# Kernel optimization log

Measured on AMD Instinct MI355X. Metric: run time of the kernel, lower is better.

The kernel has to match this reference:

```python
import jax, jax.numpy as jnp
import numpy as np


def setup_inputs() -> dict:
    key = jax.random.key(0)
    kq, kk, kv = jax.random.split(key, 3)
    B, S, D = 4, 4096, 256
    return {
        "query": jax.random.normal(kq, (B, S, D), dtype=jnp.float32),
        "key": jax.random.normal(kk, (B, S, D), dtype=jnp.float32),
        "value": jax.random.normal(kv, (B, S, D), dtype=jnp.float32),
    }


def reference(query, key, value):
    # Chunked attention with full softmax over keys per query chunk is
    # mathematically identical to standard scaled dot-product attention.
    dim = query.shape[-1]
    scale = 1.0 / jnp.sqrt(jnp.asarray(dim, query.dtype))
    scores = jnp.einsum("bqd,bkd->bqk", query, key) * scale  # (B, S, S)
    attn = jax.nn.softmax(scores, axis=-1)
    return jnp.einsum("bqk,bkd->bqd", attn, value)  # (B, S, D)
```

## Files before the change

kernel.cpp:

```cpp
#include <hip/hip_runtime.h>
#include <hip/hip_bf16.h>

#define B_ 4
#define S_ 4096
#define D_ 256
#define BM 128
#define BN 32
#define NSPLIT 4
#define SKEYS (S_/NSPLIT)
#define ITERS (SKEYS/BN)

typedef short v8s __attribute__((ext_vector_type(8)));
typedef float v16f __attribute__((ext_vector_type(16)));
typedef unsigned int v4u __attribute__((ext_vector_type(4)));

__device__ __forceinline__ unsigned short f2bf(float x){
    unsigned int u = __float_as_uint(x);
    u += 0x7fffu + ((u >> 16) & 1u);
    return (unsigned short)(u >> 16);
}
__device__ __forceinline__ unsigned int pkb(float a, float b){
    __hip_bfloat162 h = __float22bfloat162_rn(make_float2(a, b));
    union { __hip_bfloat162 h; unsigned int u; } c; c.h = h;
    return c.u;
}
__device__ __forceinline__ float bf2f(unsigned int lo16){
    return __uint_as_float(lo16 << 16);
}
__device__ __forceinline__ void gload_lds(const unsigned short* g, unsigned short* l){
    __builtin_amdgcn_global_load_lds(
        (const __attribute__((address_space(1))) unsigned int*)g,
        (__attribute__((address_space(3))) unsigned int*)l, 16, 0, 0);
}

__global__ void cvt_all(const float* __restrict__ q, const float* __restrict__ k,
                        const float* __restrict__ v,
                        uint4* __restrict__ qb, uint4* __restrict__ kb,
                        uint4* __restrict__ vt){
    __shared__ __align__(16) unsigned short lds[8192];
    int bx = blockIdx.x;
    int t  = threadIdx.x;
    int which = bx >> 9;
    int tile  = bx & 511;
    const float* srcm = (which == 0) ? q : (which == 1) ? k : v;
    const float4* src = (const float4*)(srcm + (size_t)tile * 8192);

    if (which < 2){
        const float sc = (which == 0) ? 0.09016994f : 1.0f;
        #pragma unroll
        for (int p = 0; p < 8; ++p){
            int i = p*256 + t;
            float4 a = src[i];
            int row = i >> 6, d0 = (i & 63) * 4;
            unsigned byte = (unsigned)(row*512 + d0*2) ^ (unsigned)((row & 7) << 4);
            uint2 u; u.x = pkb(a.x*sc, a.y*sc); u.y = pkb(a.z*sc, a.w*sc);
            *(uint2*)((char*)lds + byte) = u;
        }
        __syncthreads();
        uint4* dst = ((which == 0) ? qb : kb) + (size_t)tile * 1024;
        #pragma unroll
        for (int q4 = 0; q4 < 4; ++q4){
            int o = q4*256 + t;
            int c = o >> 5, row = o & 31;
            unsigned byte = (unsigned)(row*512 + c*16) ^ (unsigned)((row & 7) << 4);
            dst[o] = *(const uint4*)((const char*)lds + byte);
        }
    } else {
        #pragma unroll
        for (int p = 0; p < 8; ++p){
            int i = p*256 + t;
            float4 a = src[i];
            uint2 u; u.x = pkb(a.x, a.y); u.y = pkb(a.z, a.w);
            *(uint2*)((char*)lds + (size_t)i*8) = u;
        }
        __syncthreads();
        uint4* dst = vt + (size_t)tile * 1024;
        #pragma unroll
        for (int q4 = 0; q4 < 4; ++q4){
            union { unsigned short sh[8]; uint4 u; } cell;
            #pragma unroll
            for (int j = 0; j < 8; ++j)
                cell.sh[j] = lds[(q4*8 + j)*256 + t];
            dst[q4*256 + t] = cell.u;
        }
    }
}

__global__ __launch_bounds__(256, 2) void fa_main(
    const unsigned short* __restrict__ qb, const unsigned short* __restrict__ kb,
    const unsigned short* __restrict__ vtg,
    unsigned short* __restrict__ opart, float* __restrict__ lsep)
{
    __shared__ __align__(16) unsigned short sbuf[32768];

    int bid = blockIdx.x;
    int grp = bid & 15;
    int qt  = bid >> 4;
    int b = grp >> 2, split = grp & 3;
    int tid = threadIdx.x;
    int w = tid >> 6, lane = tid & 63, hi = lane >> 5, ln = lane & 31;

    const unsigned short* kg = (const unsigned short*)kb
                             + ((size_t)(b*128 + split*32))*8192;
    const unsigned short* vg = vtg + ((size_t)(b*128 + split*32))*8192;

    auto stageK = [&](int tile, int buf){
        const unsigned short* src = kg + (size_t)tile*8192 + w*2048;
        #pragma unroll
        for (int p = 0; p < 4; ++p)
            gload_lds(src + p*512 + lane*8, &sbuf[buf*8192 + w*2048 + p*512 + lane*8]);
    };
    auto stageV = [&](int tile, int buf){
        const unsigned short* src = vg + (size_t)tile*8192 + w*2048;
        #pragma unroll
        for (int p = 0; p < 4; ++p)
            gload_lds(src + p*512 + lane*8, &sbuf[16384 + buf*8192 + w*2048 + p*512 + lane*8]);
    };

    v8s qf[16];
    {
        const unsigned short* qsrc = qb + ((size_t)(b*128 + qt*4 + w))*8192;
        #pragma unroll
        for (int f = 0; f < 16; ++f)
            qf[f] = *(const v8s*)&qsrc[(2*f + hi)*256 + ln*8];
    }
    stageK(0, 0);
    stageV(0, 0);
    asm volatile("s_waitcnt vmcnt(0)" ::: "memory");
    __builtin_amdgcn_sched_barrier(0);
    __builtin_amdgcn_s_barrier();

    v16f oacc[8];
    #pragma unroll
    for (int t = 0; t < 8; ++t)
        #pragma unroll
        for (int r = 0; r < 16; ++r) oacc[t][r] = 0.0f;
    float l_run = 0.0f;
    v8s pf_prev[2] = {};

    for (int it = 0; it < ITERS; ++it){
        int cur = it & 1;
        const unsigned short* Kb    = &sbuf[cur*8192];
        const unsigned short* Vprev = &sbuf[16384 + (cur ^ 1)*8192];

        if (it + 1 < ITERS) stageK(it + 1, cur ^ 1);

        v16f sa, sb;
        #pragma unroll
        for (int r = 0; r < 16; ++r){ sa[r] = 0.0f; sb[r] = 0.0f; }
        __builtin_amdgcn_s_setprio(1);
        #pragma unroll
        for (int f = 0; f < 8; ++f){
            v8s a0 = *(const v8s*)&Kb[(2*f      + hi)*256 + ln*8];
            v8s a1 = *(const v8s*)&Kb[(2*(f+8) + hi)*256 + ln*8];
            sa = __builtin_amdgcn_mfma_f32_32x32x16_bf16(a0, qf[f],   sa, 0, 0, 0);
            sb = __builtin_amdgcn_mfma_f32_32x32x16_bf16(a1, qf[f+8], sb, 0, 0, 0);
        }
        __builtin_amdgcn_s_setprio(0);
        v16f sc2;
        #pragma unroll
        for (int r = 0; r < 16; ++r) sc2[r] = sa[r] + sb[r];

        if (it > 0){
            __builtin_amdgcn_s_setprio(1);
            #pragma unroll
            for (int ks = 0; ks < 2; ++ks){
                const unsigned short* vrow = &Vprev[(2*ks + hi)*2048 + ln*8];
                #pragma unroll
                for (int t2 = 0; t2 < 8; ++t2){
                    v8s av = *(const v8s*)&vrow[t2*256];
                    oacc[t2] = __builtin_amdgcn_mfma_f32_32x32x16_bf16(av, pf_prev[ks], oacc[t2], 0, 0, 0);
                }
            }
            __builtin_amdgcn_s_setprio(0);
        }

        __builtin_amdgcn_s_barrier();
        if (it + 1 < ITERS) stageV(it + 1, cur ^ 1);

        float ls = 0.0f;
        uint2 pA[4];
        #pragma unroll
        for (int c = 0; c < 4; ++c){
            float e0 = exp2f(sc2[4*c+0]), e1 = exp2f(sc2[4*c+1]);
            float e2 = exp2f(sc2[4*c+2]), e3 = exp2f(sc2[4*c+3]);
            ls += (e0 + e1) + (e2 + e3);
            pA[c].x = pkb(e0, e1); pA[c].y = pkb(e2, e3);
        }
        ls += __shfl_xor(ls, 32);
        l_run += ls;

        #pragma unroll
        for (int ks = 0; ks < 2; ++ks){
            uint2 snd = pA[2*ks + 1 - hi];
            uint2 rcv;
            rcv.x = (unsigned int)__shfl_xor((int)snd.x, 32);
            rcv.y = (unsigned int)__shfl_xor((int)snd.y, 32);
            uint2 lo = hi ? rcv : pA[2*ks];
            uint2 hb = hi ? pA[2*ks+1] : rcv;
            union { unsigned int u[4]; v8s v; } cc;
            cc.u[0] = lo.x; cc.u[1] = lo.y; cc.u[2] = hb.x; cc.u[3] = hb.y;
            pf_prev[ks] = cc.v;
        }

        if (it == ITERS - 1) asm volatile("s_waitcnt vmcnt(0)" ::: "memory");
        else                 asm volatile("s_waitcnt vmcnt(4)" ::: "memory");
        __builtin_amdgcn_sched_barrier(0);
        __builtin_amdgcn_s_barrier();
    }

    {
        const unsigned short* Vlast = &sbuf[16384 + ((ITERS - 1) & 1)*8192];
        __builtin_amdgcn_s_setprio(1);
        #pragma unroll
        for (int ks = 0; ks < 2; ++ks){
            const unsigned short* vrow = &Vlast[(2*ks + hi)*2048 + ln*8];
            #pragma unroll
            for (int t2 = 0; t2 < 8; ++t2){
                v8s av = *(const v8s*)&vrow[t2*256];
                oacc[t2] = __builtin_amdgcn_mfma_f32_32x32x16_bf16(av, pf_prev[ks], oacc[t2], 0, 0, 0);
            }
        }
        __builtin_amdgcn_s_setprio(0);
    }

    float inv = 1.0f / l_run;
    size_t orow0 = (size_t)(split*B_ + b)*S_ + qt*BM + w*32;
    if (hi == 0) lsep[orow0 + ln] = l_run;

    unsigned short* myreg = &sbuf[(w & 1) * 8320];
    #pragma unroll
    for (int rnd = 0; rnd < 2; ++rnd){
        __syncthreads();
        if ((w >> 1) == rnd){
            #pragma unroll
            for (int t = 0; t < 8; ++t)
                #pragma unroll
                for (int g = 0; g < 4; ++g){
                    uint2 u;
                    u.x = pkb(oacc[t][4*g+0]*inv, oacc[t][4*g+1]*inv);
                    u.y = pkb(oacc[t][4*g+2]*inv, oacc[t][4*g+3]*inv);
                    *(uint2*)&myreg[ln*260 + t*32 + 8*g + 4*hi] = u;
                }
            #pragma unroll
            for (int p = 0; p < 16; ++p){
                int qq = 2*p + (lane >> 5);
                int ch = lane & 31;
                v4u val = *(const v4u*)&myreg[qq*260 + ch*8];
                __builtin_nontemporal_store(val,
                    (v4u*)(opart + (orow0 + qq)*D_ + ch*8));
            }
        }
    }
}

__global__ void merge_k(const unsigned short* __restrict__ opart,
                        const float* __restrict__ lsep, float* __restrict__ out){
    int gid = blockIdx.x * 256 + threadIdx.x;
    int row = gid >> 5;
    int dc  = (gid & 31) * 8;
    float L[4];
    #pragma unroll
    for (int s = 0; s < 4; ++s) L[s] = lsep[s*(B_*S_) + row];
    float inv = 1.0f / (L[0] + L[1] + L[2] + L[3]);
    float acc[8];
    #pragma unroll
    for (int j = 0; j < 8; ++j) acc[j] = 0.0f;
    #pragma unroll
    for (int s = 0; s < 4; ++s){
        float wgt = L[s] * inv;
        uint4 u = *(const uint4*)(opart + ((size_t)(s*(B_*S_) + row))*D_ + dc);
        acc[0] += wgt * bf2f(u.x & 0xffffu);  acc[1] += wgt * bf2f(u.x >> 16);
        acc[2] += wgt * bf2f(u.y & 0xffffu);  acc[3] += wgt * bf2f(u.y >> 16);
        acc[4] += wgt * bf2f(u.z & 0xffffu);  acc[5] += wgt * bf2f(u.z >> 16);
        acc[6] += wgt * bf2f(u.w & 0xffffu);  acc[7] += wgt * bf2f(u.w >> 16);
    }
    float* op = out + (size_t)row*D_ + dc;
    *(float4*)op       = make_float4(acc[0], acc[1], acc[2], acc[3]);
    *(float4*)(op + 4) = make_float4(acc[4], acc[5], acc[6], acc[7]);
}

extern "C" void kernel_launch(void* const* d_in, const int* in_sizes, int n_in,
                              void* d_out, int out_size, void* d_ws, size_t ws_size,
                              hipStream_t stream){
    const float* q = (const float*)d_in[0];
    const float* k = (const float*)d_in[1];
    const float* v = (const float*)d_in[2];
    char* ws = (char*)d_ws;
    uint4* qb = (uint4*)(ws);
    uint4* kb = (uint4*)(ws + 8388608);
    uint4* vt = (uint4*)(ws + 16777216);
    float* lse = (float*)(ws + 25165824);
    unsigned short* opart = (unsigned short*)(ws + 25427968);

    cvt_all<<<dim3(1536), dim3(256), 0, stream>>>(q, k, v, qb, kb, vt);
    fa_main<<<dim3(512), dim3(256), 0, stream>>>((const unsigned short*)qb,
                                                 (const unsigned short*)kb,
                                                 (const unsigned short*)vt,
                                                 opart, lse);
    merge_k<<<dim3(2048), dim3(256), 0, stream>>>(opart, lse, (float*)d_out);
}
```

Baseline: 188.9 us.

## Fuse split-K merge into attention kernel via per-tile atomic counters

Drops the separate merge kernel. Splits 0-2 write bf16 partials plus their row sums, then bump a per-query-tile counter. The split-3 block spin-waits until the counter reaches 3, then combines its own registers with the three partials and writes fp32 output directly. This removes a kernel launch and one partial write/read round trip, at the cost of a memset, a spin-wait that relies on the producer blocks being co-resident or already finished, and the loss of nontemporal stores.

Result: slower. 295.9 us (+56.6%).

```diff
diff --git a/kernel.cpp b/kernel.cpp
--- a/kernel.cpp
+++ b/kernel.cpp
@@ -14,11 +14,6 @@
 typedef float v16f __attribute__((ext_vector_type(16)));
 typedef unsigned int v4u __attribute__((ext_vector_type(4)));
 
-__device__ __forceinline__ unsigned short f2bf(float x){
-    unsigned int u = __float_as_uint(x);
-    u += 0x7fffu + ((u >> 16) & 1u);
-    return (unsigned short)(u >> 16);
-}
 __device__ __forceinline__ unsigned int pkb(float a, float b){
     __hip_bfloat162 h = __float22bfloat162_rn(make_float2(a, b));
     union { __hip_bfloat162 h; unsigned int u; } c; c.h = h;
@@ -89,7 +84,8 @@
 __global__ __launch_bounds__(256, 2) void fa_main(
     const unsigned short* __restrict__ qb, const unsigned short* __restrict__ kb,
     const unsigned short* __restrict__ vtg,
-    unsigned short* __restrict__ opart, float* __restrict__ lsep)
+    unsigned short* __restrict__ opart, float* __restrict__ lsep,
+    float* __restrict__ out, unsigned int* cnt)
 {
     __shared__ __align__(16) unsigned short sbuf[32768];
 
@@ -100,8 +96,7 @@
     int tid = threadIdx.x;
     int w = tid >> 6, lane = tid & 63, hi = lane >> 5, ln = lane & 31;
 
-    const unsigned short* kg = (const unsigned short*)kb
-                             + ((size_t)(b*128 + split*32))*8192;
+    const unsigned short* kg = kb + ((size_t)(b*128 + split*32))*8192;
     const unsigned short* vg = vtg + ((size_t)(b*128 + split*32))*8192;
 
     auto stageK = [&](int tile, int buf){
@@ -198,9 +193,9 @@
             rcv.y = (unsigned int)__shfl_xor((int)snd.y, 32);
             uint2 lo = hi ? rcv : pA[2*ks];
             uint2 hb = hi ? pA[2*ks+1] : rcv;
-            union { unsigned int u[4]; v8s v; } cc;
+            union { unsigned int u[4]; v8s vv; } cc;
             cc.u[0] = lo.x; cc.u[1] = lo.y; cc.u[2] = hb.x; cc.u[3] = hb.y;
-            pf_prev[ks] = cc.v;
+            pf_prev[ks] = cc.vv;
         }
 
         if (it == ITERS - 1) asm volatile("s_waitcnt vmcnt(0)" ::: "memory");
@@ -227,57 +222,94 @@
     float inv = 1.0f / l_run;
     size_t orow0 = (size_t)(split*B_ + b)*S_ + qt*BM + w*32;
     if (hi == 0) lsep[orow0 + ln] = l_run;
+    int cidx = b*32 + qt;
 
     unsigned short* myreg = &sbuf[(w & 1) * 8320];
-    #pragma unroll
-    for (int rnd = 0; rnd < 2; ++rnd){
+
+    if (split < 3){
+        #pragma unroll
+        for (int rnd = 0; rnd < 2; ++rnd){
+            __syncthreads();
+            if ((w >> 1) == rnd){
+                #pragma unroll
+                for (int t = 0; t < 8; ++t)
+                    #pragma unroll
+                    for (int g = 0; g < 4; ++g){
+                        uint2 u;
+                        u.x = pkb(oacc[t][4*g+0]*inv, oacc[t][4*g+1]*inv);
+                        u.y = pkb(oacc[t][4*g+2]*inv, oacc[t][4*g+3]*inv);
+                        *(uint2*)&myreg[ln*260 + t*32 + 8*g + 4*hi] = u;
+                    }
+                #pragma unroll
+                for (int p = 0; p < 16; ++p){
+                    int qq = 2*p + (lane >> 5);
+                    int ch = lane & 31;
+                    v4u val = *(const v4u*)&myreg[qq*260 + ch*8];
+                    *(v4u*)(opart + (orow0 + qq)*D_ + ch*8) = val;
+                }
+            }
+        }
         __syncthreads();
-        if ((w >> 1) == rnd){
-            #pragma unroll
-            for (int t = 0; t < 8; ++t)
-                #pragma unroll
-                for (int g = 0; g < 4; ++g){
-                    uint2 u;
-                    u.x = pkb(oacc[t][4*g+0]*inv, oacc[t][4*g+1]*inv);
-                    u.y = pkb(oacc[t][4*g+2]*inv, oacc[t][4*g+3]*inv);
-                    *(uint2*)&myreg[ln*260 + t*32 + 8*g + 4*hi] = u;
+        __threadfence();
+        if (tid == 0) atomicAdd(&cnt[cidx], 1u);
+    } else {
+        if (tid == 0){
+            while (__hip_atomic_load(&cnt[cidx], __ATOMIC_ACQUIRE,
+                                     __HIP_MEMORY_SCOPE_AGENT) < 3u)
+                __builtin_amdgcn_s_sleep(2);
+        }
+        __syncthreads();
+        __threadfence();
+
+        size_t brow = (size_t)b*S_ + qt*BM + w*32;
+        #pragma unroll
+        for (int rnd = 0; rnd < 2; ++rnd){
+            __syncthreads();
+            if ((w >> 1) == rnd){
+                #pragma unroll
+                for (int t = 0; t < 8; ++t)
+                    #pragma unroll
+                    for (int g = 0; g < 4; ++g){
+                        uint2 u;
+                        u.x = pkb(oacc[t][4*g+0]*inv, oacc[t][4*g+1]*inv);
+                        u.y = pkb(oacc[t][4*g+2]*inv, oacc[t][4*g+3]*inv);
+                        *(uint2*)&myreg[ln*260 + t*32 + 8*g + 4*hi] = u;
+                    }
+                #pragma unroll
+                for (int p = 0; p < 16; ++p){
+                    int qq = 2*p + (lane >> 5);
+                    int ch = lane & 31;
+                    v4u val = *(const v4u*)&myreg[qq*260 + ch*8];
+                    size_t row = brow + qq;
+                    float L0 = lsep[row];
+                    float L1 = lsep[(size_t)(B_*S_)   + row];
+                    float L2 = lsep[(size_t)(2*B_*S_) + row];
+                    float L3 = lsep[(size_t)(3*B_*S_) + row];
+                    float winv = 1.0f / (L0 + L1 + L2 + L3);
+                    float w3 = L3 * winv;
+                    float accv[8];
+                    accv[0] = w3*bf2f(val.x & 0xffffu);  accv[1] = w3*bf2f(val.x >> 16);
+                    accv[2] = w3*bf2f(val.y & 0xffffu);  accv[3] = w3*bf2f(val.y >> 16);
+                    accv[4] = w3*bf2f(val.z & 0xffffu);  accv[5] = w3*bf2f(val.z >> 16);
+                    accv[6] = w3*bf2f(val.w & 0xffffu);  accv[7] = w3*bf2f(val.w >> 16);
+                    float Ls[3] = {L0, L1, L2};
+                    #pragma unroll
+                    for (int s = 0; s < 3; ++s){
+                        float ws = Ls[s] * winv;
+                        uint4 u = *(const uint4*)(opart
+                                  + ((size_t)s*(B_*S_) + row)*D_ + ch*8);
+                        accv[0] += ws*bf2f(u.x & 0xffffu);  accv[1] += ws*bf2f(u.x >> 16);
+                        accv[2] += ws*bf2f(u.y & 0xffffu);  accv[3] += ws*bf2f(u.y >> 16);
+                        accv[4] += ws*bf2f(u.z & 0xffffu);  accv[5] += ws*bf2f(u.z >> 16);
+                        accv[6] += ws*bf2f(u.w & 0xffffu);  accv[7] += ws*bf2f(u.w >> 16);
+                    }
+                    float* op = out + row*D_ + ch*8;
+                    *(float4*)op       = make_float4(accv[0], accv[1], accv[2], accv[3]);
+                    *(float4*)(op + 4) = make_float4(accv[4], accv[5], accv[6], accv[7]);
                 }
-            #pragma unroll
-            for (int p = 0; p < 16; ++p){
-                int qq = 2*p + (lane >> 5);
-                int ch = lane & 31;
-                v4u val = *(const v4u*)&myreg[qq*260 + ch*8];
-                __builtin_nontemporal_store(val,
-                    (v4u*)(opart + (orow0 + qq)*D_ + ch*8));
             }
         }
     }
-}
-
-__global__ void merge_k(const unsigned short* __restrict__ opart,
-                        const float* __restrict__ lsep, float* __restrict__ out){
-    int gid = blockIdx.x * 256 + threadIdx.x;
-    int row = gid >> 5;
-    int dc  = (gid & 31) * 8;
-    float L[4];
-    #pragma unroll
-    for (int s = 0; s < 4; ++s) L[s] = lsep[s*(B_*S_) + row];
-    float inv = 1.0f / (L[0] + L[1] + L[2] + L[3]);
-    float acc[8];
-    #pragma unroll
-    for (int j = 0; j < 8; ++j) acc[j] = 0.0f;
-    #pragma unroll
-    for (int s = 0; s < 4; ++s){
-        float wgt = L[s] * inv;
-        uint4 u = *(const uint4*)(opart + ((size_t)(s*(B_*S_) + row))*D_ + dc);
-        acc[0] += wgt * bf2f(u.x & 0xffffu);  acc[1] += wgt * bf2f(u.x >> 16);
-        acc[2] += wgt * bf2f(u.y & 0xffffu);  acc[3] += wgt * bf2f(u.y >> 16);
-        acc[4] += wgt * bf2f(u.z & 0xffffu);  acc[5] += wgt * bf2f(u.z >> 16);
-        acc[6] += wgt * bf2f(u.w & 0xffffu);  acc[7] += wgt * bf2f(u.w >> 16);
-    }
-    float* op = out + (size_t)row*D_ + dc;
-    *(float4*)op       = make_float4(acc[0], acc[1], acc[2], acc[3]);
-    *(float4*)(op + 4) = make_float4(acc[4], acc[5], acc[6], acc[7]);
 }
 
 extern "C" void kernel_launch(void* const* d_in, const int* in_sizes, int n_in,
@@ -291,12 +323,13 @@
     uint4* kb = (uint4*)(ws + 8388608);
     uint4* vt = (uint4*)(ws + 16777216);
     float* lse = (float*)(ws + 25165824);
-    unsigned short* opart = (unsigned short*)(ws + 25427968);
-
+    unsigned int* cnt = (unsigned int*)(ws + 25427968);
+    unsigned short* opart = (unsigned short*)(ws + 25432064);
+
+    hipMemsetAsync(cnt, 0, 4096, stream);
     cvt_all<<<dim3(1536), dim3(256), 0, stream>>>(q, k, v, qb, kb, vt);
     fa_main<<<dim3(512), dim3(256), 0, stream>>>((const unsigned short*)qb,
                                                  (const unsigned short*)kb,
                                                  (const unsigned short*)vt,
-                                                 opart, lse);
-    merge_k<<<dim3(2048), dim3(256), 0, stream>>>(opart, lse, (float*)d_out);
-}
+                                                 opart, lse, (float*)d_out, cnt);
+}
```
